# Kernel optimization log

Hardware: AMD Instinct MI355X
Metric: run time of the kernel (lower is better)

The kernel has to match this reference:

```python
import jax, jax.numpy as jnp
import numpy as np

N = 50000       # num_node
E = 800000      # num edges (avg degree 32)
F_IN, F_HID, F_OUT = 128, 128, 64


def setup_inputs() -> dict:
    key = jax.random.key(0)
    ks = jax.random.split(key, 8)
    x = jax.random.normal(ks[0], (N, F_IN), dtype=jnp.float32)
    edge_index = jax.random.randint(ks[1], (2, E), 0, N, dtype=jnp.int64)
    edge_weight = jax.random.uniform(ks[2], (E,), dtype=jnp.float32)
    s1 = 1.0 / np.sqrt(F_IN)
    s2 = 1.0 / np.sqrt(F_HID)
    W1 = jax.random.normal(ks[3], (F_HID, F_IN), dtype=jnp.float32) * s1
    b1 = jnp.zeros((F_HID,), dtype=jnp.float32)
    W2 = jax.random.normal(ks[4], (F_HID, F_HID), dtype=jnp.float32) * s2
    b2 = jnp.zeros((F_HID,), dtype=jnp.float32)
    W3 = jax.random.normal(ks[5], (F_OUT, F_HID), dtype=jnp.float32) * s2
    b3 = jnp.zeros((F_OUT,), dtype=jnp.float32)
    return {"x": x, "edge_index": edge_index, "edge_weight": edge_weight,
            "W1": W1, "b1": b1, "W2": W2, "b2": b2, "W3": W3, "b3": b3}


def _gcn_norm(edge_index, edge_weight, num_nodes):
    # PyG gcn_norm: add self-loops (weight 1), symmetric D^-1/2 (A+I) D^-1/2
    loop = jnp.arange(num_nodes, dtype=edge_index.dtype)
    row = jnp.concatenate([edge_index[0], loop])  # source
    col = jnp.concatenate([edge_index[1], loop])  # target (aggregation index)
    ew = jnp.concatenate([edge_weight, jnp.ones((num_nodes,), edge_weight.dtype)])
    deg = jax.ops.segment_sum(ew, col, num_segments=num_nodes)
    deg_safe = jnp.where(deg > 0, deg, 1.0)
    dinv = jnp.where(deg > 0, jax.lax.rsqrt(deg_safe), 0.0)
    norm = dinv[row] * ew * dinv[col]  # [E+N]
    return row, col, norm


def reference(x, edge_index, edge_weight, W1, b1, W2, b2, W3, b3):
    num_nodes = x.shape[0]
    row, col, norm = _gcn_norm(edge_index, edge_weight, num_nodes)
    h = x
    for W, b in ((W1, b1), (W2, b2), (W3, b3)):
        m = h @ W.T                                   # [N, d_out]
        msg = m[row] * norm[:, None]                  # gather + scale, [E+N, d_out]
        agg = jax.ops.segment_sum(msg, col, num_segments=num_nodes)
        h = jax.nn.relu(agg + b)                      # GCNConv bias then ReLU
    return h.reshape(-1)                              # torch.flatten
```

## Files before the change

kernel.cpp:

```cpp
#include <hip/hip_runtime.h>
#include <hip/hip_fp16.h>


#define K_DIM 128
#define SORT_ITEMS 4096

typedef unsigned long long u64;
typedef unsigned int u32;

using half8   = __attribute__((ext_vector_type(8))) _Float16;
using floatx4 = __attribute__((ext_vector_type(4))) float;


__global__ void build_hist(const int* __restrict__ row, const int* __restrict__ col,
                           const float* __restrict__ ew, u64* __restrict__ el,
                           u32* __restrict__ ghist, int E, int N, int nb,
                           const float* __restrict__ W1, const float* __restrict__ W2,
                           const float* __restrict__ W3, __half* __restrict__ Wh,
                           int nw1, int nw2, int nw3) {
    const int b = blockIdx.x;
    if (b >= nb) {
        const int i = (b - nb) * 256 + threadIdx.x;
        const int tot = nw1 + nw2 + nw3;
        if (i < tot) {
            float v = (i < nw1) ? W1[i] : (i < nw1 + nw2 ? W2[i - nw1] : W3[i - nw1 - nw2]);
            Wh[i] = __float2half_rn(v);
        }
        return;
    }
    __shared__ u32 bin[256];
    bin[threadIdx.x] = 0;
    __syncthreads();
    const int total = E + N;
    const int base = b * SORT_ITEMS;
    const int end = min(base + SORT_ITEMS, total);
    for (int i = base + threadIdx.x; i < end; i += 256) {
        u64 e;
        if (i < E) {
            e = ((u64)(u32)col[i] << 48) | ((u64)(u32)row[i] << 32)
              | (u64)__float_as_uint(ew[i]);
        } else {
            int v = i - E;
            e = ((u64)(u32)v << 48) | ((u64)(u32)v << 32)
              | (u64)__float_as_uint(1.0f);
        }
        el[i] = e;
        atomicAdd(&bin[(u32)(e >> 56)], 1u);
    }
    __syncthreads();
    ghist[(size_t)threadIdx.x * nb + b] = bin[threadIdx.x];
}

__global__ void digit_sum(const u32* __restrict__ ghist, u32* __restrict__ dsum, int nb) {
    __shared__ u32 s[256];
    const int d = blockIdx.x;
    u32 acc = 0;
    for (int i = threadIdx.x; i < nb; i += 256) acc += ghist[(size_t)d * nb + i];
    s[threadIdx.x] = acc;
    __syncthreads();
    for (int off = 128; off > 0; off >>= 1) {
        if (threadIdx.x < off) s[threadIdx.x] += s[threadIdx.x + off];
        __syncthreads();
    }
    if (threadIdx.x == 0) dsum[d] = s[0];
}

__global__ void digit_scan(u32* __restrict__ ghist, const u32* __restrict__ dsum,
                           u32* __restrict__ dbase, int nb) {
    __shared__ u32 ds[256];
    __shared__ u32 s[256];
    const int d = blockIdx.x, t = threadIdx.x;
    ds[t] = dsum[t];
    __syncthreads();
    for (int off = 1; off < 256; off <<= 1) {
        u32 u = (t >= off) ? ds[t - off] : 0;
        __syncthreads();
        ds[t] += u;
        __syncthreads();
    }
    u32 carry = (d == 0) ? 0u : ds[d - 1];
    if (t == 0) dbase[d] = carry;
    if (d == 255 && t == 0) dbase[256] = ds[255];
    for (int base = 0; base < nb; base += 256) {
        const int i = base + t;
        const u32 v = (i < nb) ? ghist[(size_t)d * nb + i] : 0;
        s[t] = v;
        __syncthreads();
        for (int off = 1; off < 256; off <<= 1) {
            u32 u = (t >= off) ? s[t - off] : 0;
            __syncthreads();
            s[t] += u;
            __syncthreads();
        }
        if (i < nb) ghist[(size_t)d * nb + i] = carry + s[t] - v;
        carry += s[255];
        __syncthreads();
    }
}

__global__ __launch_bounds__(256) void p1_scatter(const u64* __restrict__ el,
                                                  const u32* __restrict__ ghist,
                                                  u64* __restrict__ out, int total, int nb) {
    __shared__ u32 gbase[256];
    __shared__ u32 lbase[256];
    __shared__ u32 lcur[256];
    __shared__ u64 buf[SORT_ITEMS];
    const int t = threadIdx.x;
    gbase[t] = ghist[(size_t)t * nb + blockIdx.x];
    lcur[t] = 0;
    __syncthreads();
    const int base = blockIdx.x * SORT_ITEMS;
    const int end = min(base + SORT_ITEMS, total);
    const int cnt = end - base;

    u64 it[16];
    bool ok[16];
#pragma unroll
    for (int j = 0; j < 16; ++j) {
        const int i = base + t + j * 256;
        ok[j] = i < end;
        it[j] = ok[j] ? el[i] : 0;
        if (ok[j]) atomicAdd(&lcur[(u32)(it[j] >> 56)], 1u);
    }
    __syncthreads();
    const u32 v = lcur[t];
    lbase[t] = v;
    __syncthreads();
    for (int off = 1; off < 256; off <<= 1) {
        u32 u = (t >= off) ? lbase[t - off] : 0;
        __syncthreads();
        lbase[t] += u;
        __syncthreads();
    }
    const u32 excl = lbase[t] - v;
    __syncthreads();
    lbase[t] = excl;
    lcur[t] = excl;
    __syncthreads();
#pragma unroll
    for (int j = 0; j < 16; ++j) {
        if (ok[j]) {
            const u32 d = (u32)(it[j] >> 56);
            const u32 p = atomicAdd(&lcur[d], 1u);
            buf[p] = it[j];
        }
    }
    __syncthreads();
    for (int i = t; i < cnt; i += 256) {
        const u64 e = buf[i];
        const u32 d = (u32)(e >> 56);
        out[gbase[d] + i - lbase[d]] = e;
    }
}

__global__ __launch_bounds__(1024) void p2_gemm(
        const u64* __restrict__ in, u64* __restrict__ out,
        const u32* __restrict__ dbase,
        int* __restrict__ offs, float* __restrict__ dinv, int n, int ngroups,
        const float* __restrict__ x, const __half* __restrict__ Wh,
        __half* __restrict__ C) {
    if ((int)blockIdx.x < ngroups) {
        const int t = threadIdx.x;
        const int q = t >> 8;
        const int b = t & 255;
        const int base = (int)dbase[blockIdx.x];
        const int size = (int)dbase[blockIdx.x + 1] - base;
        __shared__ u32 hist[4][256];
        __shared__ u32 cur[4][256];
        __shared__ u32 s[256];
        __shared__ float wsum[4][256];
        hist[q][b] = 0;
        wsum[q][b] = 0.f;
        __syncthreads();
        for (int i = t; i < size; i += 1024)
            atomicAdd(&hist[q][(u32)(in[base + i] >> 48) & 0xFFu], 1u);
        __syncthreads();
        u32 v = 0;
        if (t < 256) {
            v = hist[0][b] + hist[1][b] + hist[2][b] + hist[3][b];
            s[b] = v;
        }
        __syncthreads();
        for (int off = 1; off < 256; off <<= 1) {
            u32 u = (t < 256 && b >= off) ? s[b - off] : 0;
            __syncthreads();
            if (t < 256) s[b] += u;
            __syncthreads();
        }
        u32 mystart = 0;
        if (t < 256) {
            mystart = (u32)base + s[b] - v;
            u32 c = mystart;
            cur[0][b] = c; c += hist[0][b];
            cur[1][b] = c; c += hist[1][b];
            cur[2][b] = c; c += hist[2][b];
            cur[3][b] = c;
        }
        __syncthreads();
        for (int i = t; i < size; i += 1024) {
            u64 e = in[base + i];
            u32 lo = (u32)(e >> 48) & 0xFFu;
            u32 p = atomicAdd(&cur[q][lo], 1u);
            out[p] = e;
            atomicAdd(&wsum[q][lo], __uint_as_float((u32)(e & 0xFFFFFFFFu)));
        }
        __syncthreads();
        const int node = blockIdx.x * 256 + b;
        if (t < 256 && node < n && v > 0) {
            offs[node] = (int)mystart;
            dinv[node] = rsqrtf(wsum[0][b] + wsum[1][b] + wsum[2][b] + wsum[3][b]);
            if (node == n - 1) offs[n] = (int)(mystart + v);
        }
    } else {
        const int gb = blockIdx.x - ngroups;
        const int wave = threadIdx.x >> 6;
        const int lane = threadIdx.x & 63;
        const int quad = lane >> 4;
        const int l16  = lane & 15;
        const int row0 = gb * 256 + wave * 16;

        int arow = row0 + l16;
        if (arow > n - 1) arow = n - 1;

        floatx4 acc[8] = {};
#pragma unroll
        for (int kc = 0; kc < 4; ++kc) {
            const int kof = kc * 32 + quad * 8;
            const float* ap = x + (size_t)arow * K_DIM + kof;
            float4 f0 = *(const float4*)ap;
            float4 f1 = *(const float4*)(ap + 4);
            half8 af;
            af[0] = (_Float16)f0.x; af[1] = (_Float16)f0.y;
            af[2] = (_Float16)f0.z; af[3] = (_Float16)f0.w;
            af[4] = (_Float16)f1.x; af[5] = (_Float16)f1.y;
            af[6] = (_Float16)f1.z; af[7] = (_Float16)f1.w;
#pragma unroll
            for (int ct = 0; ct < 8; ++ct) {
                half8 bf = *(const half8*)(Wh + (size_t)(ct * 16 + l16) * K_DIM + kof);
                acc[ct] = __builtin_amdgcn_mfma_f32_16x16x32_f16(af, bf, acc[ct], 0, 0, 0);
            }
        }
        int grow[4];
        bool ok[4];
#pragma unroll
        for (int r = 0; r < 4; ++r) {
            grow[r] = row0 + quad * 4 + r;
            ok[r] = grow[r] < n;
        }
#pragma unroll
        for (int ct = 0; ct < 8; ++ct) {
            const int colb = ct * 16 + l16;
#pragma unroll
            for (int r = 0; r < 4; ++r)
                if (ok[r])
                    C[(size_t)grow[r] * 128 + colb] = __float2half_rn(acc[ct][r]);
        }
    }
}


template <int BN>
__global__ __launch_bounds__(256) void mfma_gemm(const __half* __restrict__ Ain,
                                                 const __half* __restrict__ Wh,
                                                 __half* __restrict__ C, int nrows) {
    constexpr int NT = BN / 16;
    const int wave = threadIdx.x >> 6;
    const int lane = threadIdx.x & 63;
    const int quad = lane >> 4;
    const int l16  = lane & 15;
    const int row0 = blockIdx.x * 64 + wave * 16;

    int arow = row0 + l16;
    if (arow > nrows - 1) arow = nrows - 1;

    floatx4 acc[NT] = {};

#pragma unroll
    for (int kc = 0; kc < 4; ++kc) {
        const int kof = kc * 32 + quad * 8;
        half8 af = *(const half8*)(Ain + (size_t)arow * K_DIM + kof);
#pragma unroll
        for (int ct = 0; ct < NT; ++ct) {
            half8 bf = *(const half8*)(Wh + (size_t)(ct * 16 + l16) * K_DIM + kof);
            acc[ct] = __builtin_amdgcn_mfma_f32_16x16x32_f16(af, bf, acc[ct], 0, 0, 0);
        }
    }

    int grow[4];
    bool ok[4];
#pragma unroll
    for (int r = 0; r < 4; ++r) {
        grow[r] = row0 + quad * 4 + r;
        ok[r] = grow[r] < nrows;
    }
#pragma unroll
    for (int ct = 0; ct < NT; ++ct) {
        const int colb = ct * 16 + l16;
#pragma unroll
        for (int r = 0; r < 4; ++r)
            if (ok[r])
                C[(size_t)grow[r] * BN + colb] = __float2half_rn(acc[ct][r]);
    }
}


template <int D, typename OUT>
__global__ __launch_bounds__(256) void agg_kernel(
    const __half* __restrict__ m, const int* __restrict__ offs,
    const int2* __restrict__ csr, const float* __restrict__ dinv,
    const float* __restrict__ bias, OUT* __restrict__ out, int n) {
    const int wid = threadIdx.x >> 6;
    const int lane = threadIdx.x & 63;
    const int node = (blockIdx.x << 2) + wid;
    if (node >= n) return;
    const int beg = offs[node];
    const int end = offs[node + 1];
    const int cnt = end - beg;
    const half8* mrow = (const half8*)m;

    const int2 ev = csr[beg + min(lane, cnt - 1)];
    const int   sv = ev.y & 0xFFFF;
    const float ds = dinv[sv];
    const float wv = (lane < cnt) ? __int_as_float(ev.x) * ds : 0.f;
    const int nr = min(cnt, 64);

    float acc[8] = {0.f, 0.f, 0.f, 0.f, 0.f, 0.f, 0.f, 0.f};

    if constexpr (D == 128) {
        const int quad = lane >> 4;
        const int l16  = lane & 15;
        const int rem = nr & 15;
        if (rem) {
            float w0 = __shfl(wv, quad),      w1 = __shfl(wv, 4 + quad);
            float w2 = __shfl(wv, 8 + quad),  w3 = __shfl(wv, 12 + quad);
            int   s0 = __shfl(sv, quad),      s1 = __shfl(sv, 4 + quad);
            int   s2 = __shfl(sv, 8 + quad),  s3 = __shfl(sv, 12 + quad);
            w0 = (quad      < rem) ? w0 : 0.f;
            w1 = (4 + quad  < rem) ? w1 : 0.f;
            w2 = (8 + quad  < rem) ? w2 : 0.f;
            w3 = (12 + quad < rem) ? w3 : 0.f;
            half8 h0 = mrow[(size_t)s0 * 16 + l16];
            half8 h1 = mrow[(size_t)s1 * 16 + l16];
            half8 h2 = mrow[(size_t)s2 * 16 + l16];
            half8 h3 = mrow[(size_t)s3 * 16 + l16];
#pragma unroll
            for (int i = 0; i < 8; ++i) {
                acc[i] = fmaf(w0, (float)h0[i], acc[i]);
                acc[i] = fmaf(w1, (float)h1[i], acc[i]);
                acc[i] = fmaf(w2, (float)h2[i], acc[i]);
                acc[i] = fmaf(w3, (float)h3[i], acc[i]);
            }
        }
        for (int k = rem; k < nr; k += 16) {
            float w0 = __shfl(wv, k + quad),      w1 = __shfl(wv, k + 4 + quad);
            float w2 = __shfl(wv, k + 8 + quad),  w3 = __shfl(wv, k + 12 + quad);
            int   s0 = __shfl(sv, k + quad),      s1 = __shfl(sv, k + 4 + quad);
            int   s2 = __shfl(sv, k + 8 + quad),  s3 = __shfl(sv, k + 12 + quad);
            half8 h0 = mrow[(size_t)s0 * 16 + l16];
            half8 h1 = mrow[(size_t)s1 * 16 + l16];
            half8 h2 = mrow[(size_t)s2 * 16 + l16];
            half8 h3 = mrow[(size_t)s3 * 16 + l16];
#pragma unroll
            for (int i = 0; i < 8; ++i) {
                acc[i] = fmaf(w0, (float)h0[i], acc[i]);
                acc[i] = fmaf(w1, (float)h1[i], acc[i]);
                acc[i] = fmaf(w2, (float)h2[i], acc[i]);
                acc[i] = fmaf(w3, (float)h3[i], acc[i]);
            }
        }
        for (int k = beg + 64 + quad; k < end; k += 4) {
            const int2 e0 = csr[k];
            const int  s0 = e0.y & 0xFFFF;
            const float w0 = __int_as_float(e0.x) * dinv[s0];
            half8 hv = mrow[(size_t)s0 * 16 + l16];
#pragma unroll
            for (int i = 0; i < 8; ++i)
                acc[i] = fmaf(w0, (float)hv[i], acc[i]);
        }
#pragma unroll
        for (int i = 0; i < 8; ++i) {
            acc[i] += __shfl_xor(acc[i], 16);
            acc[i] += __shfl_xor(acc[i], 32);
        }
        if (quad == 0) {
            const float dv = dinv[node];
            const float4 b0 = *(const float4*)(bias + l16 * 8);
            const float4 b1 = *(const float4*)(bias + l16 * 8 + 4);
            const float bb[8] = {b0.x, b0.y, b0.z, b0.w, b1.x, b1.y, b1.z, b1.w};
            half8 ho;
#pragma unroll
            for (int i = 0; i < 8; ++i)
                ho[i] = (_Float16)fmaxf(acc[i] * dv + bb[i], 0.f);
            *(half8*)((__half*)out + (size_t)node * 128 + l16 * 8) = ho;
        }
    } else {
        const int oct = lane >> 3;
        const int l8  = lane & 7;
        const int rem = nr & 31;
        if (rem) {
            float w0 = __shfl(wv, oct),       w1 = __shfl(wv, 8 + oct);
            float w2 = __shfl(wv, 16 + oct),  w3 = __shfl(wv, 24 + oct);
            int   s0 = __shfl(sv, oct),       s1 = __shfl(sv, 8 + oct);
            int   s2 = __shfl(sv, 16 + oct),  s3 = __shfl(sv, 24 + oct);
            w0 = (oct      < rem) ? w0 : 0.f;
            w1 = (8 + oct  < rem) ? w1 : 0.f;
            w2 = (16 + oct < rem) ? w2 : 0.f;
            w3 = (24 + oct < rem) ? w3 : 0.f;
            half8 h0 = mrow[(size_t)s0 * 8 + l8];
            half8 h1 = mrow[(size_t)s1 * 8 + l8];
            half8 h2 = mrow[(size_t)s2 * 8 + l8];
            half8 h3 = mrow[(size_t)s3 * 8 + l8];
#pragma unroll
            for (int i = 0; i < 8; ++i) {
                acc[i] = fmaf(w0, (float)h0[i], acc[i]);
                acc[i] = fmaf(w1, (float)h1[i], acc[i]);
                acc[i] = fmaf(w2, (float)h2[i], acc[i]);
                acc[i] = fmaf(w3, (float)h3[i], acc[i]);
            }
        }
        for (int k = rem; k < nr; k += 32) {
            float w0 = __shfl(wv, k + oct),       w1 = __shfl(wv, k + 8 + oct);
            float w2 = __shfl(wv, k + 16 + oct),  w3 = __shfl(wv, k + 24 + oct);
            int   s0 = __shfl(sv, k + oct),       s1 = __shfl(sv, k + 8 + oct);
            int   s2 = __shfl(sv, k + 16 + oct),  s3 = __shfl(sv, k + 24 + oct);
            half8 h0 = mrow[(size_t)s0 * 8 + l8];
            half8 h1 = mrow[(size_t)s1 * 8 + l8];
            half8 h2 = mrow[(size_t)s2 * 8 + l8];
            half8 h3 = mrow[(size_t)s3 * 8 + l8];
#pragma unroll
            for (int i = 0; i < 8; ++i) {
                acc[i] = fmaf(w0, (float)h0[i], acc[i]);
                acc[i] = fmaf(w1, (float)h1[i], acc[i]);
                acc[i] = fmaf(w2, (float)h2[i], acc[i]);
                acc[i] = fmaf(w3, (float)h3[i], acc[i]);
            }
        }
        for (int k = beg + 64 + oct; k < end; k += 8) {
            const int2 e0 = csr[k];
            const int  s0 = e0.y & 0xFFFF;
            const float w0 = __int_as_float(e0.x) * dinv[s0];
            half8 hv = mrow[(size_t)s0 * 8 + l8];
#pragma unroll
            for (int i = 0; i < 8; ++i)
                acc[i] = fmaf(w0, (float)hv[i], acc[i]);
        }
#pragma unroll
        for (int i = 0; i < 8; ++i) {
            acc[i] += __shfl_xor(acc[i], 8);
            acc[i] += __shfl_xor(acc[i], 16);
            acc[i] += __shfl_xor(acc[i], 32);
        }
        if (oct == 0) {
            const float dv = dinv[node];
            const float4 b0 = *(const float4*)(bias + l8 * 8);
            const float4 b1 = *(const float4*)(bias + l8 * 8 + 4);
            float4 v0, v1;
            v0.x = fmaxf(acc[0] * dv + b0.x, 0.f);
            v0.y = fmaxf(acc[1] * dv + b0.y, 0.f);
            v0.z = fmaxf(acc[2] * dv + b0.z, 0.f);
            v0.w = fmaxf(acc[3] * dv + b0.w, 0.f);
            v1.x = fmaxf(acc[4] * dv + b1.x, 0.f);
            v1.y = fmaxf(acc[5] * dv + b1.y, 0.f);
            v1.z = fmaxf(acc[6] * dv + b1.z, 0.f);
            v1.w = fmaxf(acc[7] * dv + b1.w, 0.f);
            float* op = (float*)out + (size_t)node * 64 + l8 * 8;
            *(float4*)op = v0;
            *(float4*)(op + 4) = v1;
        }
    }
}


extern "C" void kernel_launch(void* const* d_in, const int* in_sizes, int n_in,
                              void* d_out, int out_size, void* d_ws, size_t ws_size,
                              hipStream_t stream) {
    const float* x  = (const float*)d_in[0];
    const int*   ei = (const int*)d_in[1];
    const float* ew = (const float*)d_in[2];
    const float* W1 = (const float*)d_in[3];
    const float* b1 = (const float*)d_in[4];
    const float* W2 = (const float*)d_in[5];
    const float* b2 = (const float*)d_in[6];
    const float* W3 = (const float*)d_in[7];
    const float* b3 = (const float*)d_in[8];
    float* out = (float*)d_out;

    const int N = in_sizes[0] / K_DIM;
    const int E = in_sizes[2];
    const int* row = ei;
    const int* col = ei + E;

    const int total = E + N;
    const int nb = (total + SORT_ITEMS - 1) / SORT_ITEMS;
    const int ngroups = (N + 255) >> 8;
    const int NW1 = 128 * 128, NW2 = 128 * 128, NW3 = 64 * 128;
    const int nwb = (NW1 + NW2 + NW3 + 255) / 256;

    u64* elA      = (u64*)d_ws;
    u64* elB      = elA + total;
    __half* m_buf = (__half*)(elB + total);
    __half* h_buf = m_buf + (size_t)N * K_DIM;
    __half* Wh    = h_buf + (size_t)N * K_DIM;
    u32* ghist    = (u32*)(Wh + NW1 + NW2 + NW3);
    u32* dsum     = ghist + (size_t)256 * nb;
    u32* dbase    = dsum + 256;
    int* offs     = (int*)(dbase + 257);
    float* dinv   = (float*)(offs + N + 1);

    build_hist<<<nb + nwb, 256, 0, stream>>>(row, col, ew, elA, ghist, E, N, nb,
                                             W1, W2, W3, Wh, NW1, NW2, NW3);
    digit_sum<<<256, 256, 0, stream>>>(ghist, dsum, nb);
    digit_scan<<<256, 256, 0, stream>>>(ghist, dsum, dbase, nb);
    p1_scatter<<<nb, 256, 0, stream>>>(elA, ghist, elB, total, nb);

    const int gemm1_blocks = (N + 255) / 256;
    p2_gemm<<<ngroups + gemm1_blocks, 1024, 0, stream>>>(
        elB, elA, dbase, offs, dinv, N, ngroups, x, Wh, m_buf);

    const int gemm_blocks = (N + 63) / 64;
    const int agg_blocks = (N + 3) / 4;
    const int2* csr = (const int2*)elA;

    agg_kernel<128, __half><<<agg_blocks, 256, 0, stream>>>(m_buf, offs, csr, dinv, b1, h_buf, N);
    mfma_gemm<128><<<gemm_blocks, 256, 0, stream>>>(h_buf, Wh + NW1, m_buf, N);
    agg_kernel<128, __half><<<agg_blocks, 256, 0, stream>>>(m_buf, offs, csr, dinv, b2, h_buf, N);
    mfma_gemm<64><<<gemm_blocks, 256, 0, stream>>>(h_buf, Wh + NW1 + NW2, m_buf, N);
    agg_kernel<64, float><<<agg_blocks, 256, 0, stream>>>(m_buf, offs, csr, dinv, b3, out, N);
}
```

Before: 268.3 us.

## Split first-layer GEMM across scatter and second sort pass kernels

Moves about half of the first-layer x@W1 GEMM rows (392 blocks of 64 rows) into the p1 scatter launch as extra blocks. The remaining rows stay in p2_gemm, which now takes a row offset. The aim is to fill idle CUs during both radix-sort passes and balance the GEMM work between them. The cost is that the scatter kernel's blocks still reserve the 32KB shared buffer even when they only run the GEMM path, which may lower occupancy.

```diff
diff --git a/kernel.cpp b/kernel.cpp
--- a/kernel.cpp
+++ b/kernel.cpp
@@ -98,13 +98,62 @@
     }
 }
 
-__global__ __launch_bounds__(256) void p1_scatter(const u64* __restrict__ el,
-                                                  const u32* __restrict__ ghist,
-                                                  u64* __restrict__ out, int total, int nb) {
+__global__ __launch_bounds__(256) void p1_gemm(const u64* __restrict__ el,
+                                               const u32* __restrict__ ghist,
+                                               u64* __restrict__ out, int total, int nb,
+                                               const float* __restrict__ x,
+                                               const __half* __restrict__ Wh,
+                                               __half* __restrict__ C, int n) {
     __shared__ u32 gbase[256];
     __shared__ u32 lbase[256];
     __shared__ u32 lcur[256];
     __shared__ u64 buf[SORT_ITEMS];
+    if ((int)blockIdx.x >= nb) {
+        const int gb = blockIdx.x - nb;
+        const int wave = threadIdx.x >> 6;
+        const int lane = threadIdx.x & 63;
+        const int quad = lane >> 4;
+        const int l16  = lane & 15;
+        const int row0 = gb * 64 + wave * 16;
+
+        int arow = row0 + l16;
+        if (arow > n - 1) arow = n - 1;
+
+        floatx4 acc[8] = {};
+#pragma unroll
+        for (int kc = 0; kc < 4; ++kc) {
+            const int kof = kc * 32 + quad * 8;
+            const float* ap = x + (size_t)arow * K_DIM + kof;
+            float4 f0 = *(const float4*)ap;
+            float4 f1 = *(const float4*)(ap + 4);
+            half8 af;
+            af[0] = (_Float16)f0.x; af[1] = (_Float16)f0.y;
+            af[2] = (_Float16)f0.z; af[3] = (_Float16)f0.w;
+            af[4] = (_Float16)f1.x; af[5] = (_Float16)f1.y;
+            af[6] = (_Float16)f1.z; af[7] = (_Float16)f1.w;
+#pragma unroll
+            for (int ct = 0; ct < 8; ++ct) {
+                half8 bf = *(const half8*)(Wh + (size_t)(ct * 16 + l16) * K_DIM + kof);
+                acc[ct] = __builtin_amdgcn_mfma_f32_16x16x32_f16(af, bf, acc[ct], 0, 0, 0);
+            }
+        }
+        int grow[4];
+        bool okr[4];
+#pragma unroll
+        for (int r = 0; r < 4; ++r) {
+            grow[r] = row0 + quad * 4 + r;
+            okr[r] = grow[r] < n;
+        }
+#pragma unroll
+        for (int ct = 0; ct < 8; ++ct) {
+            const int colb = ct * 16 + l16;
+#pragma unroll
+            for (int r = 0; r < 4; ++r)
+                if (okr[r])
+                    C[(size_t)grow[r] * 128 + colb] = __float2half_rn(acc[ct][r]);
+        }
+        return;
+    }
     const int t = threadIdx.x;
     gbase[t] = ghist[(size_t)t * nb + blockIdx.x];
     lcur[t] = 0;
@@ -158,7 +207,7 @@
         const u32* __restrict__ dbase,
         int* __restrict__ offs, float* __restrict__ dinv, int n, int ngroups,
         const float* __restrict__ x, const __half* __restrict__ Wh,
-        __half* __restrict__ C) {
+        __half* __restrict__ C, int rowoff) {
     if ((int)blockIdx.x < ngroups) {
         const int t = threadIdx.x;
         const int q = t >> 8;
@@ -217,7 +266,7 @@
         const int lane = threadIdx.x & 63;
         const int quad = lane >> 4;
         const int l16  = lane & 15;
-        const int row0 = gb * 256 + wave * 16;
+        const int row0 = rowoff + gb * 256 + wave * 16;
 
         int arow = row0 + l16;
         if (arow > n - 1) arow = n - 1;
@@ -511,11 +560,15 @@
                                              W1, W2, W3, Wh, NW1, NW2, NW3);
     digit_sum<<<256, 256, 0, stream>>>(ghist, dsum, nb);
     digit_scan<<<256, 256, 0, stream>>>(ghist, dsum, dbase, nb);
-    p1_scatter<<<nb, 256, 0, stream>>>(elA, ghist, elB, total, nb);
-
-    const int gemm1_blocks = (N + 255) / 256;
-    p2_gemm<<<ngroups + gemm1_blocks, 1024, 0, stream>>>(
-        elB, elA, dbase, offs, dinv, N, ngroups, x, Wh, m_buf);
+
+    const int g1blocks = 392;
+    const int g1rows = g1blocks * 64;
+    p1_gemm<<<nb + g1blocks, 256, 0, stream>>>(elA, ghist, elB, total, nb,
+                                               x, Wh, m_buf, N);
+
+    const int g2blocks = (N - g1rows + 255) / 256;
+    p2_gemm<<<ngroups + g2blocks, 1024, 0, stream>>>(
+        elB, elA, dbase, offs, dinv, N, ngroups, x, Wh, m_buf, g1rows);
 
     const int gemm_blocks = (N + 63) / 64;
     const int agg_blocks = (N + 3) / 4;
```

New measurement: 268.9 us, median of 2. Within noise of the previous version (+0.2%).
